# Optimization experiments

Measured on AMD Instinct MI355X. Metric: run time of the kernel, lower is better.

Reference implementation:

```python
import jax, jax.numpy as jnp
import numpy as np

D_MODEL = 1024
NUM_HEADS = 16
HEAD_DIM = D_MODEL // NUM_HEADS  # 64
B, S = 2, 2048


def setup_inputs() -> dict:
    key = jax.random.key(0)
    k1, k2, k3, k4, k5 = jax.random.split(key, 5)
    scale = 1.0 / np.sqrt(D_MODEL)
    return {
        "x": jax.random.normal(k1, (B, S, D_MODEL), dtype=jnp.float32),
        "Wq": jax.random.normal(k2, (D_MODEL, D_MODEL), dtype=jnp.float32) * scale,
        "bq": jax.random.normal(k3, (D_MODEL,), dtype=jnp.float32) * 0.02,
        "Wv": jax.random.normal(k4, (D_MODEL, D_MODEL), dtype=jnp.float32) * scale,
        "bv": jax.random.normal(k5, (D_MODEL,), dtype=jnp.float32) * 0.02,
    }


def reference(x, Wq, bq, Wv, bv):
    b, s, _ = x.shape
    d, n = HEAD_DIM, NUM_HEADS
    # nn.Linear: y = x @ W.T + b
    Q = x @ Wq.T + bq
    # NOTE (faithful to source bug): K uses the VALUE projection, key weights unused.
    KV = x @ Wv.T + bv
    # einops 'B S (d n) -> B S d n' -> 'B n S d'  (head index n is fast-varying)
    Qh = Q.reshape(b, s, d, n).transpose(0, 3, 1, 2)   # [B, n, S, d]
    Kt = KV.reshape(b, s, d, n).transpose(0, 3, 2, 1)  # [B, n, d, S]
    Vh = KV.reshape(b, s, d, n).transpose(0, 3, 1, 2)  # [B, n, S, d]
    scores = jnp.matmul(Qh, Kt) / jnp.sqrt(jnp.float32(d))  # [B, n, S, S]
    attn = jnp.matmul(jax.nn.softmax(scores, axis=-1), Vh)  # [B, n, S, d]
    # 'B n S d -> B S (n d)'
    out = attn.transpose(0, 2, 1, 3).reshape(b, s, n * d)
    return out
```

## Files before the change

kernel.cpp:

```cpp
#include <hip/hip_runtime.h>
#include <hip/hip_bf16.h>
#include <math.h>


typedef __bf16 bf16x8 __attribute__((ext_vector_type(8)));
typedef float  f32x4  __attribute__((ext_vector_type(4)));
typedef short  s16x4  __attribute__((ext_vector_type(4)));
typedef unsigned short ushort_t;
typedef unsigned short us8 __attribute__((ext_vector_type(8)));

#define QSCALE 0.1803368801111204f

__device__ __forceinline__ unsigned short f2bf(float f) {
  unsigned int u = __builtin_bit_cast(unsigned int, f);
  u += 0x7fffu + ((u >> 16) & 1u);
  return (unsigned short)(u >> 16);
}

__device__ __forceinline__ unsigned int pk2(float a, float b) {
  unsigned int ua = __builtin_bit_cast(unsigned int, a) + 0x8000u;
  unsigned int ub = __builtin_bit_cast(unsigned int, b) + 0x8000u;
  return (ua >> 16) | (ub & 0xffff0000u);
}

__device__ __forceinline__ void gl_lds16(const void* g, void* l) {
  __builtin_amdgcn_global_load_lds(
      (const __attribute__((address_space(1))) unsigned int*)g,
      (__attribute__((address_space(3))) unsigned int*)l, 16, 0, 0);
}

__device__ __forceinline__ f32x4 mfma_k32(bf16x8 a, bf16x8 b, f32x4 c) {
  return __builtin_amdgcn_mfma_f32_16x16x32_bf16(a, b, c, 0, 0, 0);
}
__device__ __forceinline__ f32x4 mfma_k16(s16x4 a, s16x4 b, f32x4 c) {
  return __builtin_amdgcn_mfma_f32_16x16x16bf16_1k(a, b, c, 0, 0, 0);
}

__global__ __launch_bounds__(256) void cvt3_kernel(const float4* __restrict__ x,
                                                   const float4* __restrict__ wq,
                                                   const float4* __restrict__ wv,
                                                   ushort4* __restrict__ dst) {
  const int i = blockIdx.x * 256 + threadIdx.x;
  const float4 v = (i < 1048576) ? x[i]
                 : (i < 1310720) ? wq[i - 1048576]
                                 : wv[i - 1310720];
  ushort4 o;
  o.x = f2bf(v.x); o.y = f2bf(v.y); o.z = f2bf(v.z); o.w = f2bf(v.w);
  dst[i] = o;
}

__global__ __launch_bounds__(256) void proj_kernel(
    const ushort_t* __restrict__ X,
    const ushort_t* __restrict__ Wqm,
    const ushort_t* __restrict__ Wvm,
    const float*    __restrict__ bq,
    const float*    __restrict__ bv,
    ushort_t* __restrict__ Qh,
    ushort_t* __restrict__ KVh)
{
  __shared__ __align__(16) unsigned char lds[32768];
  const int tid = threadIdx.x;
  const int w  = tid >> 6;
  const int l  = tid & 63;
  const int lq = l >> 4;
  const int ll = l & 15;
  const bool isQ = (blockIdx.z == 0);
  const ushort_t* Wmat = isQ ? Wqm : Wvm;
  const float*    bias = isQ ? bq  : bv;
  const int m0 = blockIdx.x * 128;
  const int by = blockIdx.y;
  const int wm = (w & 1) * 64;
  const int wn = (w >> 1) * 64;

  f32x4 acc[4][4] = {};

  for (int k0 = 0; k0 < 1024; k0 += 64) {
    __syncthreads();
#pragma unroll
    for (int t = 0; t < 4; ++t) {
      const int seg = w * 4 + t;
      const int r = seg * 8 + (l >> 3);
      const int cd = (l & 7) ^ (r & 7);
      const int cg = by * 128 + r;
      const int wrow = ((cg & 63) << 4) | (cg >> 6);
      gl_lds16(X    + (size_t)(m0 + r) * 1024 + k0 + cd * 8, lds + seg * 1024);
      gl_lds16(Wmat + (size_t)wrow * 1024 + k0 + cd * 8, lds + 16384 + seg * 1024);
    }
    __syncthreads();
#pragma unroll
    for (int kb = 0; kb < 2; ++kb) {
      const int kc = kb * 4 + lq;
      bf16x8 af[4], bfr[4];
#pragma unroll
      for (int mi = 0; mi < 4; ++mi) {
        const int m = wm + mi * 16 + ll;
        af[mi] = *(const bf16x8*)(lds + m * 128 + ((kc ^ (m & 7)) * 16));
      }
#pragma unroll
      for (int ni = 0; ni < 4; ++ni) {
        const int n = wn + ni * 16 + ll;
        bfr[ni] = *(const bf16x8*)(lds + 16384 + n * 128 + ((kc ^ (n & 7)) * 16));
      }
#pragma unroll
      for (int mi = 0; mi < 4; ++mi)
#pragma unroll
        for (int ni = 0; ni < 4; ++ni)
          acc[mi][ni] = mfma_k32(af[mi], bfr[ni], acc[mi][ni]);
    }
  }

  const int hh = (by * 128 + wn) >> 6;
#pragma unroll
  for (int ni = 0; ni < 4; ++ni) {
    const int ii = ni * 16 + ll;
    const float bb = bias[(ii << 4) | hh];
#pragma unroll
    for (int mi = 0; mi < 4; ++mi) {
#pragma unroll
      for (int r = 0; r < 4; ++r) {
        const int row = m0 + wm + mi * 16 + lq * 4 + r;
        const int b = row >> 11, s = row & 2047;
        const float v = acc[mi][ni][r] + bb;
        const size_t idx = (((size_t)(b * 16 + hh)) * 2048 + s) * 64 + ii;
        if (isQ) Qh[idx] = f2bf(v * QSCALE);
        else     KVh[idx] = f2bf(v);
      }
    }
  }
}

__global__ __launch_bounds__(256) void tr_kernel(const ushort_t* __restrict__ KVh,
                                                 ushort_t* __restrict__ KVt) {
  __shared__ __align__(16) ushort_t t[64 * 128];
  const int tid = threadIdx.x;
  const int bh = blockIdx.y;
  const int s0 = blockIdx.x * 128;
  const ushort_t* src = KVh + ((size_t)bh * 2048 + s0) * 64;
  const int d0 = (tid & 7) * 8;
#pragma unroll
  for (int u0 = 0; u0 < 64; u0 += 32) {
    const int u = u0 + (tid >> 3);
    us8 ra = *(const us8*)(src + (size_t)(2 * u) * 64 + d0);
    us8 rb = *(const us8*)(src + (size_t)(2 * u + 1) * 64 + d0);
#pragma unroll
    for (int j = 0; j < 8; ++j) {
      const int d = d0 + j;
      const int cs = (u >> 2) ^ (d & 15);
      *(unsigned int*)&t[d * 128 + cs * 8 + (u & 3) * 2] =
          (unsigned int)ra[j] | ((unsigned int)rb[j] << 16);
    }
  }
  __syncthreads();
  ushort_t* dst = KVt + (size_t)bh * 64 * 2048 + s0;
  const int d = tid >> 2;
#pragma unroll
  for (int p = 0; p < 4; ++p) {
    const int c = (tid & 3) + p * 4;
    const int cs = c ^ (d & 15);
    us8 v = *(const us8*)&t[d * 128 + cs * 8];
    *(us8*)(dst + (size_t)d * 2048 + c * 8) = v;
  }
}

__global__ __launch_bounds__(256, 2) void attn_kernel(
    const ushort_t* __restrict__ Qh,
    const ushort_t* __restrict__ KVh,
    const ushort_t* __restrict__ KVt,
    float* __restrict__ out)
{
  __shared__ __align__(16) unsigned char sm[65536];
  const int tid = threadIdx.x;
  const int w  = tid >> 6;
  const int l  = tid & 63;
  const int quad = l >> 4;
  const int ll = l & 15;
  const int bid = blockIdx.x;
  const int bh = ((bid & 7) << 2) | (bid >> 7);
  const int qt = (bid >> 3) & 15;
  const int b = bh >> 4, h = bh & 15;
  const int qbase = qt * 128 + w * 32;
  const ushort_t* Qhead  = Qh  + (size_t)bh * (2048 * 64);
  const ushort_t* Khead  = KVh + (size_t)bh * (2048 * 64);
  const ushort_t* Vthead = KVt + (size_t)bh * (64 * 2048);

  bf16x8 qf[2][2];
#pragma unroll
  for (int c = 0; c < 2; ++c)
#pragma unroll
    for (int kb = 0; kb < 2; ++kb)
      qf[c][kb] = *(const bf16x8*)(Qhead + (size_t)(qbase + c * 16 + ll) * 64 +
                                   kb * 32 + quad * 8);

  const int ksegr = (w * 4) * 8 + (l >> 3);
  const int kcd   = (l & 7);
#pragma unroll
  for (int t = 0; t < 4; ++t) {
    const int seg = w * 4 + t;
    const int r = seg * 8 + (l >> 3);
    const int cd = (l & 7) ^ (r & 7);
    gl_lds16(Khead + (size_t)r * 64 + cd * 8, sm + seg * 1024);
  }
#pragma unroll
  for (int t = 0; t < 4; ++t) {
    const int seg = w * 4 + t;
    const int d = seg * 4 + (l >> 4);
    const int k16 = ((l & 15) - 2 * d) & 15;
    gl_lds16(Vthead + (size_t)d * 2048 + k16 * 8, sm + 32768 + seg * 1024);
  }

  f32x4 O[2][4] = {};
  float l_run[2] = {0.f, 0.f};

  for (int kt = 0; kt < 16; ++kt) {
    const int sk0 = kt * 128;
    const int buf = kt & 1;
    __syncthreads();

    if (kt < 15) {
      const int bo = (buf ^ 1) * 16384;
#pragma unroll
      for (int t = 0; t < 4; ++t) {
        const int seg = w * 4 + t;
        const int r = seg * 8 + (l >> 3);
        const int cd = (l & 7) ^ (r & 7);
        gl_lds16(Khead + (size_t)(sk0 + 128 + r) * 64 + cd * 8, sm + bo + seg * 1024);
      }
#pragma unroll
      for (int t = 0; t < 4; ++t) {
        const int seg = w * 4 + t;
        const int d = seg * 4 + (l >> 4);
        const int k16 = ((l & 15) - 2 * d) & 15;
        gl_lds16(Vthead + (size_t)d * 2048 + sk0 + 128 + k16 * 8,
                 sm + 32768 + bo + seg * 1024);
      }
    }
    const unsigned char* Kb = sm + buf * 16384;
    const unsigned char* Vb = sm + 32768 + buf * 16384;

    f32x4 Sa[2][8] = {};
#pragma unroll
    for (int kb = 0; kb < 2; ++kb) {
      const int kc = kb * 4 + quad;
#pragma unroll
      for (int ni = 0; ni < 8; ++ni) {
        const int n = ni * 16 + ll;
        const bf16x8 ak = *(const bf16x8*)(Kb + n * 128 + ((kc ^ (n & 7)) * 16));
        Sa[0][ni] = mfma_k32(ak, qf[0][kb], Sa[0][ni]);
        Sa[1][ni] = mfma_k32(ak, qf[1][kb], Sa[1][ni]);
      }
    }

    s16x4 pk[2][8];
#pragma unroll
    for (int c = 0; c < 2; ++c) {
      float ps = 0.f;
#pragma unroll
      for (int ni = 0; ni < 8; ++ni) {
        const float p0 = __builtin_amdgcn_exp2f(Sa[c][ni][0]);
        const float p1 = __builtin_amdgcn_exp2f(Sa[c][ni][1]);
        const float p2 = __builtin_amdgcn_exp2f(Sa[c][ni][2]);
        const float p3 = __builtin_amdgcn_exp2f(Sa[c][ni][3]);
        ps += (p0 + p1) + (p2 + p3);
        const uint2 uu = make_uint2(pk2(p0, p1), pk2(p2, p3));
        pk[c][ni] = __builtin_bit_cast(s16x4, uu);
      }
      ps += __shfl_xor(ps, 16);
      ps += __shfl_xor(ps, 32);
      l_run[c] += ps;
    }

#pragma unroll
    for (int ni = 0; ni < 8; ++ni) {
#pragma unroll
      for (int no = 0; no < 4; ++no) {
        const int d = no * 16 + ll;
        const s16x4 bv = *(const s16x4*)(Vb + d * 256 +
                                         ((4 * ni + quad + 4 * ll) & 31) * 8);
        O[0][no] = mfma_k16(pk[0][ni], bv, O[0][no]);
        O[1][no] = mfma_k16(pk[1][ni], bv, O[1][no]);
      }
    }
  }
  (void)ksegr; (void)kcd;

#pragma unroll
  for (int c = 0; c < 2; ++c) {
    const float inv = 1.f / l_run[c];
    float invr[4];
#pragma unroll
    for (int r = 0; r < 4; ++r)
      invr[r] = __shfl(inv, (l & 48) + ((l & 48) >> 2) + r);
    float* op = out + ((size_t)(b * 2048) + qbase + c * 16) * 1024 + h * 64;
#pragma unroll
    for (int no = 0; no < 4; ++no)
#pragma unroll
      for (int r = 0; r < 4; ++r) {
        const int q = quad * 4 + r;
        op[(size_t)q * 1024 + no * 16 + ll] = O[c][no][r] * invr[r];
      }
  }
}

extern "C" void kernel_launch(void* const* d_in, const int* in_sizes, int n_in,
                              void* d_out, int out_size, void* d_ws, size_t ws_size,
                              hipStream_t stream) {
  const float* x  = (const float*)d_in[0];
  const float* Wq = (const float*)d_in[1];
  const float* bq = (const float*)d_in[2];
  const float* Wv = (const float*)d_in[3];
  const float* bv = (const float*)d_in[4];
  float* out = (float*)d_out;
  char* ws = (char*)d_ws;

  ushort_t* xbf  = (ushort_t*)(ws);
  ushort_t* wqbf = (ushort_t*)(ws + 8388608);
  ushort_t* wvbf = (ushort_t*)(ws + 10485760);
  ushort_t* Qh   = (ushort_t*)(ws + 12582912);
  ushort_t* KVh  = (ushort_t*)(ws + 20971520);
  ushort_t* KVt  = (ushort_t*)(ws + 29360128);

  cvt3_kernel<<<6144, 256, 0, stream>>>((const float4*)x, (const float4*)Wq,
                                        (const float4*)Wv, (ushort4*)xbf);
  proj_kernel<<<dim3(32, 8, 2), 256, 0, stream>>>(xbf, wqbf, wvbf, bq, bv, Qh, KVh);
  tr_kernel<<<dim3(16, 32), 256, 0, stream>>>(KVh, KVt);
  attn_kernel<<<512, 256, 0, stream>>>(Qh, KVh, KVt, out);
}
```

Before: 162.8 us.

## Load V fragments directly from global into registers instead of LDS staging

Removes the double-buffered LDS staging of the transposed V tile and has each wave read its V operand fragments straight from global memory into registers, split into two halves issued around the QK^T and softmax phases. This halves shared memory use, which may allow more resident blocks, and drops LDS write/read traffic for V. In exchange, each of the four waves redundantly fetches the same V data from global/L2 with narrow 8-byte loads, and register pressure rises from holding 32 extra fragments.

```diff
diff --git a/kernel.cpp b/kernel.cpp
--- a/kernel.cpp
+++ b/kernel.cpp
@@ -168,7 +168,7 @@
     const ushort_t* __restrict__ KVt,
     float* __restrict__ out)
 {
-  __shared__ __align__(16) unsigned char sm[65536];
+  __shared__ __align__(16) unsigned char sm[32768];
   const int tid = threadIdx.x;
   const int w  = tid >> 6;
   const int l  = tid & 63;
@@ -191,8 +191,6 @@
       qf[c][kb] = *(const bf16x8*)(Qhead + (size_t)(qbase + c * 16 + ll) * 64 +
                                    kb * 32 + quad * 8);
 
-  const int ksegr = (w * 4) * 8 + (l >> 3);
-  const int kcd   = (l & 7);
 #pragma unroll
   for (int t = 0; t < 4; ++t) {
     const int seg = w * 4 + t;
@@ -200,24 +198,16 @@
     const int cd = (l & 7) ^ (r & 7);
     gl_lds16(Khead + (size_t)r * 64 + cd * 8, sm + seg * 1024);
   }
-#pragma unroll
-  for (int t = 0; t < 4; ++t) {
-    const int seg = w * 4 + t;
-    const int d = seg * 4 + (l >> 4);
-    const int k16 = ((l & 15) - 2 * d) & 15;
-    gl_lds16(Vthead + (size_t)d * 2048 + k16 * 8, sm + 32768 + seg * 1024);
-  }
 
   f32x4 O[2][4] = {};
   float l_run[2] = {0.f, 0.f};
 
   for (int kt = 0; kt < 16; ++kt) {
     const int sk0 = kt * 128;
-    const int buf = kt & 1;
     __syncthreads();
 
     if (kt < 15) {
-      const int bo = (buf ^ 1) * 16384;
+      const int bo = ((kt + 1) & 1) * 16384;
 #pragma unroll
       for (int t = 0; t < 4; ++t) {
         const int seg = w * 4 + t;
@@ -225,17 +215,16 @@
         const int cd = (l & 7) ^ (r & 7);
         gl_lds16(Khead + (size_t)(sk0 + 128 + r) * 64 + cd * 8, sm + bo + seg * 1024);
       }
-#pragma unroll
-      for (int t = 0; t < 4; ++t) {
-        const int seg = w * 4 + t;
-        const int d = seg * 4 + (l >> 4);
-        const int k16 = ((l & 15) - 2 * d) & 15;
-        gl_lds16(Vthead + (size_t)d * 2048 + sk0 + 128 + k16 * 8,
-                 sm + 32768 + bo + seg * 1024);
-      }
-    }
-    const unsigned char* Kb = sm + buf * 16384;
-    const unsigned char* Vb = sm + 32768 + buf * 16384;
+    }
+    const unsigned char* Kb = sm + (kt & 1) * 16384;
+
+    s16x4 vfA[4][4];
+#pragma unroll
+    for (int ni = 0; ni < 4; ++ni)
+#pragma unroll
+      for (int no = 0; no < 4; ++no)
+        vfA[ni][no] = *(const s16x4*)(Vthead + (size_t)(no * 16 + ll) * 2048 +
+                                      sk0 + ni * 16 + quad * 4);
 
     f32x4 Sa[2][8] = {};
 #pragma unroll
@@ -249,6 +238,14 @@
         Sa[1][ni] = mfma_k32(ak, qf[1][kb], Sa[1][ni]);
       }
     }
+
+    s16x4 vfB[4][4];
+#pragma unroll
+    for (int ni = 0; ni < 4; ++ni)
+#pragma unroll
+      for (int no = 0; no < 4; ++no)
+        vfB[ni][no] = *(const s16x4*)(Vthead + (size_t)(no * 16 + ll) * 2048 +
+                                      sk0 + 64 + ni * 16 + quad * 4);
 
     s16x4 pk[2][8];
 #pragma unroll
@@ -273,15 +270,12 @@
     for (int ni = 0; ni < 8; ++ni) {
 #pragma unroll
       for (int no = 0; no < 4; ++no) {
-        const int d = no * 16 + ll;
-        const s16x4 bv = *(const s16x4*)(Vb + d * 256 +
-                                         ((4 * ni + quad + 4 * ll) & 31) * 8);
+        const s16x4 bv = (ni < 4) ? vfA[ni][no] : vfB[ni - 4][no];
         O[0][no] = mfma_k16(pk[0][ni], bv, O[0][no]);
         O[1][no] = mfma_k16(pk[1][ni], bv, O[1][no]);
       }
     }
   }
-  (void)ksegr; (void)kcd;
 
 #pragma unroll
   for (int c = 0; c < 2; ++c) {
```

Result: slower. 229.0 us (+40.6%).
